# Kernel optimization log

Hardware: AMD Instinct MI355X
Metric: run time of the kernel (lower is better)

Reference implementation:

```python
import jax, jax.numpy as jnp
import numpy as np


def setup_inputs() -> dict:
    key = jax.random.key(0)
    k1, k2, k3, k4 = jax.random.split(key, 4)
    B, Tv, Ta, D = 8, 2048, 2048, 256
    return {
        "visual_features": jax.random.normal(k1, (B, Tv, D), dtype=jnp.float32),
        "audio_features": jax.random.normal(k2, (B, Ta, D), dtype=jnp.float32),
        "visual_weights": jax.random.uniform(k3, (D, D), dtype=jnp.float32),
        "audio_weights": jax.random.uniform(k4, (D, D), dtype=jnp.float32),
        "num_neighbors": 8,
    }


def _pairwise_l2(vm, am):
    # ||v - a|| via the expanded form to avoid the [B,Tv,Ta,D] intermediate.
    sq = (
        jnp.sum(vm * vm, -1)[:, :, None]
        + jnp.sum(am * am, -1)[:, None, :]
        - 2.0 * jnp.einsum("btd,bsd->bts", vm, am)
    )
    sq = jnp.maximum(sq, 0.0)
    # safe sqrt: subgradient 0 at 0 (matches torch.norm backward convention)
    return jnp.where(sq > 0, jnp.sqrt(jnp.where(sq > 0, sq, 1.0)), 0.0)


def reference(visual_features, audio_features, visual_weights, audio_weights, num_neighbors):
    vm = visual_features @ visual_weights  # [B,Tv,D]
    am = audio_features @ audio_weights    # [B,Ta,D]
    graph = jnp.exp(-_pairwise_l2(vm, am))  # [B,Tv,Ta]
    # topk over the visual axis (dim=1): move it last for lax.top_k
    _, idx = jax.lax.top_k(jnp.swapaxes(graph, 1, 2), num_neighbors)  # [B,Ta,k]
    idx = jnp.swapaxes(idx, 1, 2)  # [B,k,Ta]
    # broadcasted gather along axis 1: result [B,k,Ta,D]
    vn = jnp.take_along_axis(visual_features[:, :, None, :], idx[..., None], axis=1)
    an = jnp.take_along_axis(audio_features[:, :, None, :], idx[..., None], axis=1)
    # mean over dim=2 (the Ta axis of the gathered neighbors) -> [B,k,D]
    return vn.mean(axis=2), an.mean(axis=2)
```

## Files before the change

### kernel.cpp

```cpp
#include <hip/hip_runtime.h>
#include <cstddef>
#include <cstdint>

namespace {
constexpr int kB   = 8;
constexpr int kT   = 2048;
constexpr int kD   = 256;
constexpr int kK   = 8;
constexpr int kM   = kB * kT;
constexpr int kNC  = kB * kT;
constexpr int kColCap = 64;
constexpr int kOvCap  = 1 << 17;
constexpr int kStr = 264;
constexpr float kMinNormalF = 1.17549435e-38f;
}

typedef __attribute__((ext_vector_type(8)))  __bf16 bf16x8;
typedef __attribute__((ext_vector_type(16))) float  f32x16;

__device__ inline unsigned short f2bf_rne(float x) {
  unsigned u = __float_as_uint(x);
  unsigned r = (u + 0x7FFFu + ((u >> 16) & 1u)) >> 16;
  return (unsigned short)r;
}
__device__ inline float bf2f(unsigned short h) {
  return __uint_as_float((unsigned)h << 16);
}
union FragU { uint4 u4; bf16x8 v; };

__device__ inline void async16(const unsigned short* g, unsigned short* l) {
  __builtin_amdgcn_global_load_lds(
      (const __attribute__((address_space(1))) unsigned int*)(const void*)g,
      (__attribute__((address_space(3))) unsigned int*)(void*)l, 16, 0, 0);
}

__device__ inline void stage_tile_async(const unsigned short* src,
                                        unsigned short* S, int w, int lane) {
  const int hi = lane >> 5, lo = lane & 31;
#pragma unroll
  for (int i = 0; i < 8; ++i) {
    const int p = w * 8 + i;
    const int rowl = p * 2 + hi;
    const int c = lo ^ (rowl & 31);
    async16(src + (size_t)rowl * kD + c * 8, S + p * 512);
  }
}
__device__ inline uint4 lds_frag(const unsigned short* S, int row, int kc, int half) {
  const int c = (kc * 2 + half) ^ (row & 31);
  return *reinterpret_cast<const uint4*>(S + row * 256 + c * 8);
}

__global__ __launch_bounds__(256) void prep(const float* __restrict__ W0,
                                            const float* __restrict__ W1,
                                            unsigned short* __restrict__ T0,
                                            unsigned short* __restrict__ T1,
                                            unsigned* __restrict__ zeroBase,
                                            int zeroWords,
                                            unsigned* __restrict__ outW) {
  const int blk = blockIdx.x;
  if (blk < 128) {
    const float* W = (blk & 64) ? W1 : W0;
    unsigned short* WT = (blk & 64) ? T1 : T0;
    const int t = blk & 63;
    const int c0 = (t & 7) * 32, k0 = (t >> 3) * 32;
    __shared__ float tile[32][33];
    const int tx = threadIdx.x & 31, ty = threadIdx.x >> 5;
#pragma unroll
    for (int i = 0; i < 4; ++i)
      tile[ty + i * 8][tx] = W[(size_t)(k0 + ty + i * 8) * kD + c0 + tx];
    __syncthreads();
#pragma unroll
    for (int i = 0; i < 4; ++i)
      WT[(size_t)(c0 + ty + i * 8) * kD + k0 + tx] = f2bf_rne(tile[tx][ty + i * 8]);
  } else {
    for (int i = (blk - 128) * 256 + threadIdx.x; i < zeroWords; i += 32 * 256)
      zeroBase[i] = 0u;
    for (int i = (blk - 128) * 256 + threadIdx.x; i < 2 * kB * kK * kD; i += 32 * 256)
      outW[i] = 0u;
  }
}

__global__ __launch_bounds__(256) void gemm_hyb(const float* __restrict__ Xv,
                                                const float* __restrict__ Xa,
                                                const unsigned short* __restrict__ WvT,
                                                const unsigned short* __restrict__ WaT,
                                                unsigned short* __restrict__ Cv,
                                                unsigned short* __restrict__ Ca,
                                                float* __restrict__ nv,
                                                float* __restrict__ na) {
  __shared__ unsigned short S[64 * kStr];
  const int z = blockIdx.z;
  const float* X = z ? Xa : Xv;
  const unsigned short* WT = z ? WaT : WvT;
  unsigned short* Cb = z ? Ca : Cv;
  float* nrm = z ? na : nv;
  const int r0 = blockIdx.x * 64;
  const int tid = threadIdx.x;
  const int w = tid >> 6, lane = tid & 63;
  const int wt = w & 1, wc = w >> 1;
  const int half = lane >> 5, ln = lane & 31;

#pragma unroll
  for (int i = 0; i < 16; ++i) {
    const int idx = i * 256 + tid;
    const int row = idx >> 6, g = idx & 63;
    const float4 v = *reinterpret_cast<const float4*>(X + (size_t)(r0 + row) * kD + g * 4);
    ushort4 o;
    o.x = f2bf_rne(v.x); o.y = f2bf_rne(v.y); o.z = f2bf_rne(v.z); o.w = f2bf_rne(v.w);
    *reinterpret_cast<ushort4*>(S + row * kStr + g * 4) = o;
  }
  __syncthreads();
  uint4 afr[16];
#pragma unroll
  for (int kc = 0; kc < 16; ++kc)
    afr[kc] = *reinterpret_cast<const uint4*>(S + (wt * 32 + ln) * kStr + kc * 16 + half * 8);

  float ns[16];
#pragma unroll
  for (int r = 0; r < 16; ++r) ns[r] = 0.0f;

  for (int ct = 0; ct < 4; ++ct) {
    const int c0 = ct * 64;
    __syncthreads();
    stage_tile_async(WT + (size_t)c0 * kD, S, w, lane);
    __syncthreads();
    f32x16 acc;
#pragma unroll
    for (int i = 0; i < 16; ++i) acc[i] = 0.0f;
#pragma unroll
    for (int kc = 0; kc < 16; ++kc) {
      FragU fa, fb;
      fa.u4 = afr[kc];
      fb.u4 = lds_frag(S, wc * 32 + ln, kc, half);
      acc = __builtin_amdgcn_mfma_f32_32x32x16_bf16(fa.v, fb.v, acc, 0, 0, 0);
    }
    const int col = c0 + wc * 32 + ln;
#pragma unroll
    for (int r = 0; r < 16; ++r) {
      const int row = r0 + wt * 32 + (r & 3) + 8 * (r >> 2) + 4 * half;
      const unsigned short us = f2bf_rne(acc[r]);
      Cb[(size_t)row * kD + col] = us;
      const float f = bf2f(us);
      ns[r] += f * f;
    }
  }
#pragma unroll
  for (int r = 0; r < 16; ++r) {
    float v = ns[r];
#pragma unroll
    for (int off = 1; off < 32; off <<= 1) v += __shfl_xor(v, off, 64);
    if (ln == 0) {
      const int row = r0 + wt * 32 + (r & 3) + 8 * (r >> 2) + 4 * half;
      atomicAdd(nrm + row, v);
    }
  }
}

__global__ __launch_bounds__(256) void keys_v14(const unsigned short* __restrict__ vmb,
                                                const unsigned short* __restrict__ amb,
                                                const float* __restrict__ vn2,
                                                const float* __restrict__ an2,
                                                unsigned* __restrict__ colCount,
                                                uint2* __restrict__ colRecs,
                                                unsigned* __restrict__ ovCount,
                                                uint2* __restrict__ ovRecs) {
  __shared__ unsigned short S[64 * 256];
  const int b = blockIdx.z;
  const int t0 = blockIdx.x * 128;
  const int sr0 = blockIdx.y * 256;
  const int tid = threadIdx.x;
  const int w = tid >> 6, lane = tid & 63;
  const int half = lane >> 5, ln = lane & 31;

  uint4 afr[16];
#pragma unroll
  for (int h = 0; h < 2; ++h) {
    __syncthreads();
    stage_tile_async(vmb + ((size_t)b * kT + t0 + h * 64) * kD, S, w, lane);
    __syncthreads();
    if ((w >> 1) == h) {
#pragma unroll
      for (int kc = 0; kc < 16; ++kc)
        afr[kc] = lds_frag(S, (w & 1) * 32 + ln, kc, half);
    }
  }

  const float* v2p = vn2 + (size_t)b * kT + t0 + w * 32;

  for (int st = 0; st < 4; ++st) {
    const int s0 = sr0 + st * 64;
    __syncthreads();
    stage_tile_async(amb + ((size_t)b * kT + s0) * kD, S, w, lane);
    __syncthreads();
    f32x16 acc[2];
#pragma unroll
    for (int j = 0; j < 2; ++j)
#pragma unroll
      for (int i = 0; i < 16; ++i) acc[j][i] = 0.0f;
#pragma unroll
    for (int kc = 0; kc < 16; ++kc) {
      FragU fa; fa.u4 = afr[kc];
#pragma unroll
      for (int ss = 0; ss < 2; ++ss) {
        FragU fb;
        fb.u4 = lds_frag(S, ss * 32 + ln, kc, half);
        acc[ss] = __builtin_amdgcn_mfma_f32_32x32x16_bf16(fa.v, fb.v, acc[ss], 0, 0, 0);
      }
    }
    float a2s[2];
#pragma unroll
    for (int ss = 0; ss < 2; ++ss)
      a2s[ss] = an2[(size_t)b * kT + s0 + ss * 32 + ln];
#pragma unroll
    for (int g = 0; g < 4; ++g) {
      const float4 v2 = *reinterpret_cast<const float4*>(v2p + g * 8 + half * 4);
      const float v2a[4] = {v2.x, v2.y, v2.z, v2.w};
#pragma unroll
      for (int ss = 0; ss < 2; ++ss) {
        const int s = s0 + ss * 32 + ln;
        const float a2 = a2s[ss];
        const int c = (b << 11) | s;
#pragma unroll
        for (int q = 0; q < 4; ++q) {
          const float raw = v2a[q] + a2 - 2.0f * acc[ss][4 * g + q];
          if (raw < 7744.0f) {
            const float dist = sqrtf(fmaxf(raw, 0.0f));
            const float e = expf(-dist);
            if (e >= kMinNormalF) {
              const int t = t0 + w * 32 + g * 8 + half * 4 + q;
              const unsigned slot = atomicAdd(&colCount[c], 1u);
              if (slot < (unsigned)kColCap) {
                colRecs[(size_t)c * kColCap + slot] = make_uint2(__float_as_uint(e), (unsigned)t);
              } else {
                const unsigned pos = ((unsigned)b << 22) | ((unsigned)s << 11) | (unsigned)t;
                const unsigned oi = atomicAdd(ovCount, 1u);
                if (oi < (unsigned)kOvCap) ovRecs[oi] = make_uint2(__float_as_uint(e), pos);
              }
            }
          }
        }
      }
    }
  }
}

__global__ __launch_bounds__(256) void gather_fused(const float* __restrict__ visual,
                                                    const float* __restrict__ audio,
                                                    const unsigned* __restrict__ colCount,
                                                    const uint2* __restrict__ colRecs,
                                                    const unsigned* __restrict__ ovCount,
                                                    const uint2* __restrict__ ovRecs,
                                                    float* __restrict__ out) {
  __shared__ int sIdx[32];
  const int u = blockIdx.x;
  const int bj = u >> 6, ch = u & 63;
  const int b = bj >> 3, j = bj & 7;
  const int tid = threadIdx.x;
  if (tid < 32) {
    const int s = ch * 32 + tid;
    const int c = (b << 11) | s;
    unsigned K[8]; int T[8];
#pragma unroll
    for (int i = 0; i < 8; ++i) { K[i] = 0u; T[i] = 0x7FFFFFFF; }
    const int cnt = (int)colCount[c];
    const int m = min(cnt, kColCap);
    for (int i = 0; i < m; ++i) {
      const uint2 r = colRecs[(size_t)c * kColCap + i];
      const unsigned kx = r.x; const int tx = (int)r.y;
      if (kx > K[7] || (kx == K[7] && tx < T[7])) {
        K[7] = kx; T[7] = tx;
#pragma unroll
        for (int q = 7; q >= 1; --q) {
          const bool sw = (K[q] > K[q - 1]) || (K[q] == K[q - 1] && T[q] < T[q - 1]);
          if (sw) {
            const unsigned tk = K[q]; K[q] = K[q - 1]; K[q - 1] = tk;
            const int tt = T[q];      T[q] = T[q - 1]; T[q - 1] = tt;
          }
        }
      }
    }
    if (cnt > kColCap) {
      int n = (int)*ovCount;
      if (n > kOvCap) n = kOvCap;
      for (int i = 0; i < n; ++i) {
        const uint2 r = ovRecs[i];
        if ((int)(r.y >> 11) == c) {
          const unsigned kx = r.x; const int tx = (int)(r.y & 2047u);
          if (kx > K[7] || (kx == K[7] && tx < T[7])) {
            K[7] = kx; T[7] = tx;
#pragma unroll
            for (int q = 7; q >= 1; --q) {
              const bool sw = (K[q] > K[q - 1]) || (K[q] == K[q - 1] && T[q] < T[q - 1]);
              if (sw) {
                const unsigned tk = K[q]; K[q] = K[q - 1]; K[q - 1] = tk;
                const int tt = T[q];      T[q] = T[q - 1]; T[q - 1] = tt;
              }
            }
          }
        }
      }
    }
    int mcnt = 0;
#pragma unroll
    for (int i = 0; i < 8; ++i) if (K[i] > 0u) mcnt++;
    int outv[8];
#pragma unroll
    for (int i = 0; i < 8; ++i) outv[i] = T[i];
    int cand = 0;
    for (int r = mcnt; r < 8; ++r) {
      bool taken = true;
      while (taken) {
        taken = false;
#pragma unroll
        for (int q = 0; q < 8; ++q)
          if (q < mcnt && T[q] == cand) taken = true;
        if (taken) cand++;
      }
      outv[r] = cand++;
    }
    sIdx[tid] = outv[j];
  }
  __syncthreads();
  float accV = 0.f, accA = 0.f;
  for (int i = 0; i < 32; ++i) {
    const int t = sIdx[i];
    const size_t base = ((size_t)b * kT + t) * kD + tid;
    accV += visual[base];
    accA += audio[base];
  }
  atomicAdd(&out[(size_t)bj * kD + tid], accV * (1.0f / kT));
  atomicAdd(&out[(size_t)kB * kK * kD + (size_t)bj * kD + tid], accA * (1.0f / kT));
}

extern "C" void kernel_launch(void* const* d_in, const int* in_sizes, int n_in,
                              void* d_out, int out_size, void* d_ws, size_t ws_size,
                              hipStream_t stream) {
  (void)in_sizes; (void)n_in; (void)out_size; (void)ws_size;
  const float* visual = (const float*)d_in[0];
  const float* audio  = (const float*)d_in[1];
  const float* Wv     = (const float*)d_in[2];
  const float* Wa     = (const float*)d_in[3];
  float* out = (float*)d_out;

  char* ws = (char*)d_ws;
  unsigned short* WvT = (unsigned short*)ws;
  unsigned short* WaT = WvT + (size_t)kD * kD;
  unsigned short* vmb = WaT + (size_t)kD * kD;
  unsigned short* amb = vmb + (size_t)kM * kD;
  float* vn2 = (float*)(amb + (size_t)kM * kD);
  float* an2 = vn2 + kM;
  unsigned* colCount = (unsigned*)(an2 + kM);
  unsigned* ovCount  = colCount + kNC;
  uint2* colRecs = (uint2*)(ovCount + 8);
  uint2* ovRecs  = colRecs + (size_t)kNC * kColCap;
  const int zeroWords = 2 * kM + kNC + 8;

  prep<<<dim3(160), 256, 0, stream>>>(Wv, Wa, WvT, WaT, (unsigned*)vn2, zeroWords,
                                      (unsigned*)out);
  gemm_hyb<<<dim3(kM / 64, 1, 2), 256, 0, stream>>>(visual, audio, WvT, WaT,
                                                    vmb, amb, vn2, an2);
  keys_v14<<<dim3(kT / 128, kT / 256, kB), 256, 0, stream>>>(vmb, amb, vn2, an2,
                                                             colCount, colRecs, ovCount, ovRecs);
  gather_fused<<<dim3(4096), 256, 0, stream>>>(visual, audio, colCount, colRecs,
                                               ovCount, ovRecs, out);
}
```

Baseline: 152.3 us.

## Double-buffer LDS tiles in GEMM and distance kernels, remap block order

Both the projection GEMM and the pairwise-distance kernel now keep two LDS tile buffers, so the async stage of the next weight or audio tile runs while MFMAs work on the current one. This also removes one barrier per iteration. The distance kernel additionally remaps the linear block index so that consecutive hardware blocks come from different batches or tiles, which is meant to spread L2/HBM traffic. The cost is doubled LDS per block, which may reduce occupancy.

Result: no change. 150.1 us (-1.5%).

```diff
diff --git a/kernel.cpp b/kernel.cpp
--- a/kernel.cpp
+++ b/kernel.cpp
@@ -88,7 +88,9 @@
                                                 unsigned short* __restrict__ Ca,
                                                 float* __restrict__ nv,
                                                 float* __restrict__ na) {
-  __shared__ unsigned short S[64 * kStr];
+  __shared__ unsigned short S[64 * kStr + 64 * 256];
+  unsigned short* bufA = S;
+  unsigned short* bufB = S + 64 * kStr;
   const int z = blockIdx.z;
   const float* X = z ? Xa : Xv;
   const unsigned short* WT = z ? WaT : WvT;
@@ -107,23 +109,27 @@
     const float4 v = *reinterpret_cast<const float4*>(X + (size_t)(r0 + row) * kD + g * 4);
     ushort4 o;
     o.x = f2bf_rne(v.x); o.y = f2bf_rne(v.y); o.z = f2bf_rne(v.z); o.w = f2bf_rne(v.w);
-    *reinterpret_cast<ushort4*>(S + row * kStr + g * 4) = o;
-  }
-  __syncthreads();
+    *reinterpret_cast<ushort4*>(bufA + row * kStr + g * 4) = o;
+  }
+  __syncthreads();
+
+  stage_tile_async(WT, bufB, w, lane);
   uint4 afr[16];
 #pragma unroll
   for (int kc = 0; kc < 16; ++kc)
-    afr[kc] = *reinterpret_cast<const uint4*>(S + (wt * 32 + ln) * kStr + kc * 16 + half * 8);
+    afr[kc] = *reinterpret_cast<const uint4*>(bufA + (wt * 32 + ln) * kStr + kc * 16 + half * 8);
+  __syncthreads();
 
   float ns[16];
 #pragma unroll
   for (int r = 0; r < 16; ++r) ns[r] = 0.0f;
 
   for (int ct = 0; ct < 4; ++ct) {
+    unsigned short* cur = (ct & 1) ? bufA : bufB;
+    unsigned short* nxt = (ct & 1) ? bufB : bufA;
+    if (ct < 3)
+      stage_tile_async(WT + (size_t)(ct + 1) * 64 * kD, nxt, w, lane);
     const int c0 = ct * 64;
-    __syncthreads();
-    stage_tile_async(WT + (size_t)c0 * kD, S, w, lane);
-    __syncthreads();
     f32x16 acc;
 #pragma unroll
     for (int i = 0; i < 16; ++i) acc[i] = 0.0f;
@@ -131,7 +137,7 @@
     for (int kc = 0; kc < 16; ++kc) {
       FragU fa, fb;
       fa.u4 = afr[kc];
-      fb.u4 = lds_frag(S, wc * 32 + ln, kc, half);
+      fb.u4 = lds_frag(cur, wc * 32 + ln, kc, half);
       acc = __builtin_amdgcn_mfma_f32_32x32x16_bf16(fa.v, fb.v, acc, 0, 0, 0);
     }
     const int col = c0 + wc * 32 + ln;
@@ -143,6 +149,7 @@
       const float f = bf2f(us);
       ns[r] += f * f;
     }
+    if (ct < 3) __syncthreads();
   }
 #pragma unroll
   for (int r = 0; r < 16; ++r) {
@@ -156,7 +163,7 @@
   }
 }
 
-__global__ __launch_bounds__(256) void keys_v14(const unsigned short* __restrict__ vmb,
+__global__ __launch_bounds__(256) void keys_v15(const unsigned short* __restrict__ vmb,
                                                 const unsigned short* __restrict__ amb,
                                                 const float* __restrict__ vn2,
                                                 const float* __restrict__ an2,
@@ -164,34 +171,38 @@
                                                 uint2* __restrict__ colRecs,
                                                 unsigned* __restrict__ ovCount,
                                                 uint2* __restrict__ ovRecs) {
-  __shared__ unsigned short S[64 * 256];
-  const int b = blockIdx.z;
-  const int t0 = blockIdx.x * 128;
-  const int sr0 = blockIdx.y * 256;
+  __shared__ unsigned short S[2][64 * 256];
+  const int hw = blockIdx.x + (blockIdx.y << 4) + (blockIdx.z << 7);
+  const int lg = ((hw & 7) << 7) | (hw >> 3);
+  const int b = lg >> 7;
+  const int t0 = (lg & 15) << 7;
+  const int sr0 = ((lg >> 4) & 7) << 8;
   const int tid = threadIdx.x;
   const int w = tid >> 6, lane = tid & 63;
   const int half = lane >> 5, ln = lane & 31;
 
+  stage_tile_async(vmb + ((size_t)b * kT + t0) * kD, S[0], w, lane);
+  stage_tile_async(vmb + ((size_t)b * kT + t0 + 64) * kD, S[1], w, lane);
+  __syncthreads();
   uint4 afr[16];
-#pragma unroll
-  for (int h = 0; h < 2; ++h) {
-    __syncthreads();
-    stage_tile_async(vmb + ((size_t)b * kT + t0 + h * 64) * kD, S, w, lane);
-    __syncthreads();
-    if ((w >> 1) == h) {
-#pragma unroll
-      for (int kc = 0; kc < 16; ++kc)
-        afr[kc] = lds_frag(S, (w & 1) * 32 + ln, kc, half);
-    }
-  }
+  {
+    const unsigned short* Sa = S[w >> 1];
+#pragma unroll
+    for (int kc = 0; kc < 16; ++kc)
+      afr[kc] = lds_frag(Sa, (w & 1) * 32 + ln, kc, half);
+  }
+  __syncthreads();
+
+  stage_tile_async(amb + ((size_t)b * kT + sr0) * kD, S[0], w, lane);
+  __syncthreads();
 
   const float* v2p = vn2 + (size_t)b * kT + t0 + w * 32;
 
   for (int st = 0; st < 4; ++st) {
     const int s0 = sr0 + st * 64;
-    __syncthreads();
-    stage_tile_async(amb + ((size_t)b * kT + s0) * kD, S, w, lane);
-    __syncthreads();
+    const int cur = st & 1;
+    if (st < 3)
+      stage_tile_async(amb + ((size_t)b * kT + s0 + 64) * kD, S[cur ^ 1], w, lane);
     f32x16 acc[2];
 #pragma unroll
     for (int j = 0; j < 2; ++j)
@@ -203,7 +214,7 @@
 #pragma unroll
       for (int ss = 0; ss < 2; ++ss) {
         FragU fb;
-        fb.u4 = lds_frag(S, ss * 32 + ln, kc, half);
+        fb.u4 = lds_frag(S[cur], ss * 32 + ln, kc, half);
         acc[ss] = __builtin_amdgcn_mfma_f32_32x32x16_bf16(fa.v, fb.v, acc[ss], 0, 0, 0);
       }
     }
@@ -241,6 +252,7 @@
         }
       }
     }
+    if (st < 3) __syncthreads();
   }
 }
 
@@ -359,7 +371,7 @@
                                       (unsigned*)out);
   gemm_hyb<<<dim3(kM / 64, 1, 2), 256, 0, stream>>>(visual, audio, WvT, WaT,
                                                     vmb, amb, vn2, an2);
-  keys_v14<<<dim3(kT / 128, kT / 256, kB), 256, 0, stream>>>(vmb, amb, vn2, an2,
+  keys_v15<<<dim3(kT / 128, kT / 256, kB), 256, 0, stream>>>(vmb, amb, vn2, an2,
                                                              colCount, colRecs, ovCount, ovRecs);
   gather_fused<<<dim3(4096), 256, 0, stream>>>(visual, audio, colCount, colRecs,
                                                ovCount, ovRecs, out);
```
